# Kernel tuning notes

Hardware: AMD Instinct MI355X
Metric: run time of the kernel (lower is better)

The kernel has to match this reference:

```python
import jax, jax.numpy as jnp
import numpy as np

T, B, IN, H, L = 512, 256, 64, 128, 5  # seq, batch, in_dim, hidden, layers


def _lstm_layer(x_seq, W_ih, W_hh, b_ih, b_hh):
    # x_seq: [T, B, D]; W_ih: [4H, D]; W_hh: [4H, H]; biases: [4H]
    # Precompute input contribution for all timesteps (big GEMM, compute-dense)
    pre = jnp.einsum('tbd,gd->tbg', x_seq, W_ih) + b_ih + b_hh  # [T, B, 4H]
    h0 = jnp.zeros((x_seq.shape[1], W_hh.shape[1]), x_seq.dtype)
    c0 = h0

    def step(carry, p):
        h, c = carry
        gates = p + h @ W_hh.T  # [B, 4H], PyTorch gate order i,f,g,o
        i, f, g, o = jnp.split(gates, 4, axis=-1)
        i = jax.nn.sigmoid(i)
        f = jax.nn.sigmoid(f)
        g = jnp.tanh(g)
        o = jax.nn.sigmoid(o)
        c = f * c + i * g
        h = o * jnp.tanh(c)
        return (h, c), h

    _, hs = jax.lax.scan(step, (h0, c0), pre)
    return hs  # [T, B, H]


def setup_inputs() -> dict:
    key = jax.random.key(0)
    ks = jax.random.split(key, 6)
    s = 1.0 / np.sqrt(H)  # PyTorch LSTM init scale
    return {
        'x': jax.random.normal(ks[0], (T, B, IN), jnp.float32),
        'W_ih0': jax.random.uniform(ks[1], (4 * H, IN), jnp.float32, -s, s),
        'W_ih_rest': jax.random.uniform(ks[2], (L - 1, 4 * H, H), jnp.float32, -s, s),
        'W_hh': jax.random.uniform(ks[3], (L, 4 * H, H), jnp.float32, -s, s),
        'b_ih': jax.random.uniform(ks[4], (L, 4 * H), jnp.float32, -s, s),
        'b_hh': jax.random.uniform(ks[5], (L, 4 * H), jnp.float32, -s, s),
    }


def reference(x, W_ih0, W_ih_rest, W_hh, b_ih, b_hh):
    # 5-layer stacked LSTM, eval mode (inter-layer dropout inactive).
    h = _lstm_layer(x, W_ih0, W_hh[0], b_ih[0], b_hh[0])
    for l in range(1, L):  # fixed small layer loop
        h = _lstm_layer(h, W_ih_rest[l - 1], W_hh[l], b_ih[l], b_hh[l])
    return h  # [T, B, H]
```

## Files before the change

### kernel.cpp

```cpp
#include <hip/hip_runtime.h>


typedef unsigned short ushort_t;
typedef unsigned int uint_t;
typedef unsigned long long ull_t;
typedef __attribute__((ext_vector_type(8))) short short8;
typedef __attribute__((ext_vector_type(4))) float floatx4;
typedef __attribute__((ext_vector_type(2))) float floatx2;

#define T_STEPS 512
#define BATCH   256
#define HID     128
#define NL      5
#define NBG     16
#define RING_R  64
#define PRIME   24
#define FLAG_STRIDE 16
#define SLOT_U  (BATCH * HID / 2)
#define RING_U  ((size_t)RING_R * SLOT_U)
#define WS_NEED (8192 + 4 * RING_U * 4)
#define LDS_BYTES 98304

__device__ __forceinline__ ushort_t f2bf(float f) {
  unsigned int u = __float_as_uint(f);
  u += 0x7FFF + ((u >> 16) & 1);
  return (ushort_t)(u >> 16);
}
__device__ __forceinline__ float sigm(float x) {
  float e = __builtin_amdgcn_exp2f(-1.442695041f * x);
  return __builtin_amdgcn_rcpf(1.0f + e);
}
__device__ __forceinline__ float tanh_(float x) {
  float e = __builtin_amdgcn_exp2f(-2.885390082f * x);
  float s = __builtin_amdgcn_rcpf(1.0f + e);
  return __builtin_fmaf(2.0f, s, -1.0f);
}
__device__ __forceinline__ int flag_ld(const int* p) {
  return __hip_atomic_load(p, __ATOMIC_RELAXED, __HIP_MEMORY_SCOPE_AGENT);
}
__device__ __forceinline__ ull_t ring_ld8(const uint_t* base, int tid) {
  return __hip_atomic_load((const ull_t*)base + tid, __ATOMIC_RELAXED,
                           __HIP_MEMORY_SCOPE_AGENT);
}
__device__ __forceinline__ void ring_st8(uint_t* base, int tid, ull_t v) {
  __hip_atomic_store((ull_t*)base + tid, v, __ATOMIC_RELAXED,
                     __HIP_MEMORY_SCOPE_AGENT);
}

__global__ void init_flags(int* flags) {
  int i = blockIdx.x * 256 + threadIdx.x;
  if (i < NL * NBG * FLAG_STRIDE)
    __hip_atomic_store(&flags[i], 0, __ATOMIC_RELAXED,
                       __HIP_MEMORY_SCOPE_AGENT);
}

template <int KIN, bool SRC_F32, bool RING_OUT>
__device__ __forceinline__ void lstm_stage(
    unsigned char* lds,
    const float* xf32,
    const uint_t* ring_in,
    const float* __restrict__ Wih, const float* __restrict__ Whh,
    const float* __restrict__ bih, const float* __restrict__ bhh,
    uint_t* ring_out,
    float* out_f32,
    int* up_flag, int* down_flag, int* my_flag, int bg)
{
  constexpr int KX = KIN / 32, KT = KX + 4;
  constexpr int XS = KIN + 8;
  constexpr int HS = 128 + 8;

  typedef ushort_t (*XT)[16][XS];
  typedef ushort_t (*HT)[16][HS];
  XT Xr = (XT)lds;
  HT Hr = (HT)(lds + (size_t)8 * 16 * XS * 2);
  int* upm = (int*)(lds + (size_t)8 * 16 * XS * 2 + (size_t)2 * 16 * HS * 2);
  int* dnm = upm + 4;

  const int tid  = threadIdx.x;
  const int wave = tid >> 6;
  const int lane = tid & 63;
  const int col  = lane & 15;
  const int quad = lane >> 4;
  const int j    = wave * 16 + col;
  const int frow = tid >> 5;
  const int fc   = tid & 31;

  for (int i = tid; i < 2 * 16 * HS; i += 512) (&Hr[0][0][0])[i] = 0;
  if (tid == 0) {
#pragma unroll
    for (int i = 0; i < 4; ++i) { upm[i] = 0; dnm[i] = 0; }
  }

  short8 wf[4][KT];
#pragma unroll
  for (int nt = 0; nt < 4; ++nt) {
    int n = nt * 128 + j;
#pragma unroll
    for (int kt = 0; kt < KX; ++kt) {
      const float* p = Wih + n * KIN + kt * 32 + quad * 8;
      short8 w;
#pragma unroll
      for (int e = 0; e < 8; ++e) w[e] = (short)f2bf(p[e]);
      wf[nt][kt] = w;
    }
#pragma unroll
    for (int kt = 0; kt < 4; ++kt) {
      const float* p = Whh + n * 128 + kt * 32 + quad * 8;
      short8 w;
#pragma unroll
      for (int e = 0; e < 8; ++e) w[e] = (short)f2bf(p[e]);
      wf[nt][KX + kt] = w;
    }
  }
  const float bi  = bih[j]       + bhh[j];
  const float bf_ = bih[128 + j] + bhh[128 + j];
  const float bgi = bih[256 + j] + bhh[256 + j];
  const float bo  = bih[384 + j] + bhh[384 + j];

  floatx4 c = {0.f, 0.f, 0.f, 0.f};
  int pu = 0, pd = 0;
  ull_t  pf4[4];
  floatx2 px4[4];
  floatx4 pA[4], pB[4];

  __syncthreads();

  if constexpr (!SRC_F32) {
    int v = 0;
    while ((v = flag_ld(up_flag)) < PRIME) __builtin_amdgcn_s_sleep(1);
    asm volatile("" ::: "memory");
    if (tid == 0) {
#pragma unroll
      for (int i = 0; i < 4; ++i) upm[i] = v;
      pu = v;
    }
    ull_t pr[8];
#pragma unroll
    for (int s = 0; s < 8; ++s)
      pr[s] = ring_ld8(ring_in + (size_t)s * SLOT_U + bg * 1024, tid);
#pragma unroll
    for (int s = 0; s < 8; ++s)
      *(ull_t*)(&Xr[s][frow][fc * 4]) = pr[s];
  } else {
    floatx2 pr[8];
#pragma unroll
    for (int s = 0; s < 8; ++s)
      pr[s] = *(const floatx2*)(xf32 +
                                ((size_t)s * BATCH + bg * 16 + frow) * 64 +
                                fc * 2);
#pragma unroll
    for (int s = 0; s < 8; ++s)
      *(uint_t*)(&Xr[s][frow][fc * 2]) =
          (uint_t)f2bf(pr[s][0]) | ((uint_t)f2bf(pr[s][1]) << 16);
  }
  asm volatile("s_waitcnt lgkmcnt(0)\n\ts_barrier" ::: "memory");

  pA[0] = (floatx4){bi, bi, bi, bi};
  pA[1] = (floatx4){bf_, bf_, bf_, bf_};
  pA[2] = (floatx4){bgi, bgi, bgi, bgi};
  pA[3] = (floatx4){bo, bo, bo, bo};
#pragma unroll
  for (int kt = 0; kt < KX; ++kt) {
    short8 ax = *(const short8*)(&Xr[0][col][kt * 32 + quad * 8]);
    pA[0] = __builtin_amdgcn_mfma_f32_16x16x32_bf16(ax, wf[0][kt], pA[0], 0, 0, 0);
    pA[1] = __builtin_amdgcn_mfma_f32_16x16x32_bf16(ax, wf[1][kt], pA[1], 0, 0, 0);
    pA[2] = __builtin_amdgcn_mfma_f32_16x16x32_bf16(ax, wf[2][kt], pA[2], 0, 0, 0);
    pA[3] = __builtin_amdgcn_mfma_f32_16x16x32_bf16(ax, wf[3][kt], pA[3], 0, 0, 0);
  }

  auto body = [&](int t, floatx4 (&pc)[4], floatx4 (&pn)[4]) {
    if ((t & 3) == 0) {
      if (t >= 4) {
        asm volatile("s_waitcnt vmcnt(0)\n\ts_barrier" ::: "memory");
        if (tid == 0)
          __hip_atomic_store(my_flag, t - 1, __ATOMIC_RELAXED,
                             __HIP_MEMORY_SCOPE_AGENT);
#pragma unroll
        for (int g = 0; g < 4; ++g) {
          const int s = t + 4 + g;
          if (s < T_STEPS) {
            if constexpr (SRC_F32)
              *(uint_t*)(&Xr[s & 7][frow][fc * 2]) =
                  (uint_t)f2bf(px4[g][0]) | ((uint_t)f2bf(px4[g][1]) << 16);
            else
              *(ull_t*)(&Xr[s & 7][frow][fc * 4]) = pf4[g];
          }
        }
      }
      if (t + 8 < T_STEPS) {
        if constexpr (!SRC_F32) {
          int need = t + 12;
          if (need > T_STEPS) need = T_STEPS;
          if (upm[t & 3] < need) {
            while (flag_ld(up_flag) < need) __builtin_amdgcn_s_sleep(1);
          }
        }
        asm volatile("" ::: "memory");
#pragma unroll
        for (int g = 0; g < 4; ++g) {
          const int s = t + 8 + g;
          if (s < T_STEPS) {
            if constexpr (SRC_F32)
              px4[g] = *(const floatx2*)(
                  xf32 + ((size_t)s * BATCH + bg * 16 + frow) * 64 + fc * 2);
            else
              pf4[g] = ring_ld8(
                  ring_in + (size_t)(s & (RING_R - 1)) * SLOT_U + bg * 1024,
                  tid);
          }
        }
      }
    }
    const int dn = dnm[t & 3];

    if constexpr (RING_OUT) {
      if (t >= 1) {
        const int s = t - 1;
        if (s - dn > RING_R - 16) {
          while (s - flag_ld(down_flag) > RING_R - 16)
            __builtin_amdgcn_s_sleep(1);
          asm volatile("" ::: "memory");
        }
        ull_t h8 = *(const ull_t*)(&Hr[t & 1][frow][fc * 4]);
        ring_st8(ring_out + (size_t)(s & (RING_R - 1)) * SLOT_U + bg * 1024,
                 tid, h8);
      }
    }

#pragma unroll
    for (int kt = 0; kt < 4; ++kt) {
      short8 a = *(const short8*)(&Hr[t & 1][col][kt * 32 + quad * 8]);
      pc[0] = __builtin_amdgcn_mfma_f32_16x16x32_bf16(a, wf[0][KX + kt], pc[0], 0, 0, 0);
      pc[1] = __builtin_amdgcn_mfma_f32_16x16x32_bf16(a, wf[1][KX + kt], pc[1], 0, 0, 0);
      pc[2] = __builtin_amdgcn_mfma_f32_16x16x32_bf16(a, wf[2][KX + kt], pc[2], 0, 0, 0);
      pc[3] = __builtin_amdgcn_mfma_f32_16x16x32_bf16(a, wf[3][KX + kt], pc[3], 0, 0, 0);
    }

    if (t + 1 < T_STEPS) {
      pn[0] = (floatx4){bi, bi, bi, bi};
      pn[1] = (floatx4){bf_, bf_, bf_, bf_};
      pn[2] = (floatx4){bgi, bgi, bgi, bgi};
      pn[3] = (floatx4){bo, bo, bo, bo};
#pragma unroll
      for (int kt = 0; kt < KX; ++kt) {
        short8 ax = *(const short8*)(&Xr[(t + 1) & 7][col][kt * 32 + quad * 8]);
        pn[0] = __builtin_amdgcn_mfma_f32_16x16x32_bf16(ax, wf[0][kt], pn[0], 0, 0, 0);
        pn[1] = __builtin_amdgcn_mfma_f32_16x16x32_bf16(ax, wf[1][kt], pn[1], 0, 0, 0);
        pn[2] = __builtin_amdgcn_mfma_f32_16x16x32_bf16(ax, wf[2][kt], pn[2], 0, 0, 0);
        pn[3] = __builtin_amdgcn_mfma_f32_16x16x32_bf16(ax, wf[3][kt], pn[3], 0, 0, 0);
      }
    }

    if (tid == 0) {
      if constexpr (!SRC_F32) {
        upm[(t + 2) & 3] = pu;
        pu = flag_ld(up_flag);
      }
      if constexpr (RING_OUT) {
        dnm[(t + 2) & 3] = pd;
        pd = flag_ld(down_flag);
      }
    }

    ushort_t (*wr)[HS] = Hr[(t & 1) ^ 1];
#pragma unroll
    for (int r = 0; r < 4; ++r) {
      float iv = sigm(pc[0][r]);
      float fv = sigm(pc[1][r]);
      float gv = tanh_(pc[2][r]);
      float ov = sigm(pc[3][r]);
      float cn = __builtin_fmaf(fv, c[r], iv * gv);
      c[r] = cn;
      float hv = ov * tanh_(cn);
      wr[quad * 4 + r][j] = f2bf(hv);
      if constexpr (!RING_OUT) {
        out_f32[((size_t)t * BATCH + bg * 16 + quad * 4 + r) * HID + j] = hv;
      }
    }

    asm volatile("s_waitcnt lgkmcnt(0)\n\ts_barrier" ::: "memory");
  };

  for (int t = 0; t < T_STEPS; t += 2) {
    body(t, pA, pB);
    body(t + 1, pB, pA);
  }

  if constexpr (RING_OUT) {
    const int s = T_STEPS - 1;
    while (s - flag_ld(down_flag) > RING_R - 16) __builtin_amdgcn_s_sleep(1);
    asm volatile("" ::: "memory");
    ull_t h8 = *(const ull_t*)(&Hr[T_STEPS & 1][frow][fc * 4]);
    ring_st8(ring_out + (size_t)(s & (RING_R - 1)) * SLOT_U + bg * 1024, tid,
             h8);
  }
  asm volatile("s_waitcnt vmcnt(0)\n\ts_barrier" ::: "memory");
  if (tid == 0)
    __hip_atomic_store(my_flag, T_STEPS, __ATOMIC_RELAXED,
                       __HIP_MEMORY_SCOPE_AGENT);
}

__global__ __launch_bounds__(512) void lstm_pipe(
    const float* x, const float* Wih0, const float* WihR,
    const float* Whh, const float* bih, const float* bhh,
    float* out, uint_t* ring, int* flags)
{
  __shared__ __align__(16) unsigned char lds_raw[LDS_BYTES];
  const int l  = blockIdx.x >> 4;
  const int bg = blockIdx.x & 15;
  int* mine = flags + (l * NBG + bg) * FLAG_STRIDE;
  int* up   = (l > 0) ? flags + ((l - 1) * NBG + bg) * FLAG_STRIDE : nullptr;
  int* down = (l < 4) ? flags + ((l + 1) * NBG + bg) * FLAG_STRIDE : nullptr;

  if (l == 0) {
    lstm_stage<64, true, true>(lds_raw, x, nullptr, Wih0, Whh, bih, bhh,
                               ring, nullptr, up, down, mine, bg);
  } else if (l < 4) {
    lstm_stage<128, false, true>(lds_raw, nullptr,
                                 ring + (size_t)(l - 1) * RING_U,
                                 WihR + (size_t)(l - 1) * 512 * 128,
                                 Whh + (size_t)l * 512 * 128,
                                 bih + l * 512, bhh + l * 512,
                                 ring + (size_t)l * RING_U, nullptr,
                                 up, down, mine, bg);
  } else {
    lstm_stage<128, false, false>(lds_raw, nullptr,
                                  ring + (size_t)3 * RING_U,
                                  WihR + (size_t)3 * 512 * 128,
                                  Whh + (size_t)4 * 512 * 128,
                                  bih + 4 * 512, bhh + 4 * 512,
                                  nullptr, out, up, nullptr, mine, bg);
  }
}

template <int KIN>
__global__ __launch_bounds__(512) void lstm_layer(
    const float* xin, float* hout,
    const float* __restrict__ Wih, const float* __restrict__ Whh,
    const float* __restrict__ bih, const float* __restrict__ bhh)
{
  constexpr int KX = KIN / 32, KT = KX + 4;
  constexpr int AW = KIN + 128, AS = AW + 8;
  constexpr int NSTG = 16 * KIN / 4;

  const int bg = blockIdx.x, tid = threadIdx.x;
  const int wave = tid >> 6, lane = tid & 63;
  const int col = lane & 15, quad = lane >> 4;
  const int j = wave * 16 + col;

  __shared__ __align__(16) ushort_t Ah[2][16][AS];
  for (int i = tid; i < 2 * 16 * AS; i += 512) (&Ah[0][0][0])[i] = 0;

  short8 wf[4][KT];
#pragma unroll
  for (int nt = 0; nt < 4; ++nt) {
    int n = nt * 128 + j;
#pragma unroll
    for (int kt = 0; kt < KX; ++kt) {
      const float* p = Wih + n * KIN + kt * 32 + quad * 8;
      short8 w;
#pragma unroll
      for (int e = 0; e < 8; ++e) w[e] = (short)f2bf(p[e]);
      wf[nt][kt] = w;
    }
#pragma unroll
    for (int kt = 0; kt < 4; ++kt) {
      const float* p = Whh + n * 128 + kt * 32 + quad * 8;
      short8 w;
#pragma unroll
      for (int e = 0; e < 8; ++e) w[e] = (short)f2bf(p[e]);
      wf[nt][KX + kt] = w;
    }
  }
  const float bi  = bih[j]       + bhh[j];
  const float bf_ = bih[128 + j] + bhh[128 + j];
  const float bgi = bih[256 + j] + bhh[256 + j];
  const float bo  = bih[384 + j] + bhh[384 + j];

  floatx4 c = {0.f, 0.f, 0.f, 0.f};
  const int srow = tid / (KIN / 4), scol = (tid % (KIN / 4)) * 4;
  floatx4 xv = {0.f, 0.f, 0.f, 0.f};
  auto stage_load = [&](int t) {
    if (tid < NSTG && t < T_STEPS)
      xv = *(const floatx4*)(xin + (size_t)(t * BATCH + bg * 16 + srow) * KIN + scol);
  };
  auto stage_store = [&](int t, ushort_t (*buf)[AS]) {
    if (tid < NSTG && t < T_STEPS) {
#pragma unroll
      for (int e = 0; e < 4; ++e) buf[srow][scol + e] = f2bf(xv[e]);
    }
  };
  __syncthreads();
  stage_load(0); stage_store(0, Ah[0]); stage_load(1);
  __syncthreads();

  for (int t = 0; t < T_STEPS; ++t) {
    ushort_t (*rd)[AS] = Ah[t & 1];
    ushort_t (*wr)[AS] = Ah[(t & 1) ^ 1];
    short8 af[KT];
#pragma unroll
    for (int kt = 0; kt < KT; ++kt)
      af[kt] = *(const short8*)(&rd[col][kt * 32 + quad * 8]);
    floatx4 a0 = {0, 0, 0, 0}, a1 = {0, 0, 0, 0}, a2 = {0, 0, 0, 0},
            a3 = {0, 0, 0, 0};
#pragma unroll
    for (int kt = 0; kt < KT; ++kt) {
      short8 a = af[kt];
      a0 = __builtin_amdgcn_mfma_f32_16x16x32_bf16(a, wf[0][kt], a0, 0, 0, 0);
      a1 = __builtin_amdgcn_mfma_f32_16x16x32_bf16(a, wf[1][kt], a1, 0, 0, 0);
      a2 = __builtin_amdgcn_mfma_f32_16x16x32_bf16(a, wf[2][kt], a2, 0, 0, 0);
      a3 = __builtin_amdgcn_mfma_f32_16x16x32_bf16(a, wf[3][kt], a3, 0, 0, 0);
    }
    stage_store(t + 1, wr);
    stage_load(t + 2);
    size_t obase = (size_t)(t * BATCH + bg * 16) * HID + j;
#pragma unroll
    for (int r = 0; r < 4; ++r) {
      int row = quad * 4 + r;
      float iv = sigm(a0[r] + bi);
      float fv = sigm(a1[r] + bf_);
      float gv = tanh_(a2[r] + bgi);
      float ov = sigm(a3[r] + bo);
      float cn = __builtin_fmaf(fv, c[r], iv * gv);
      c[r] = cn;
      float hv = ov * tanh_(cn);
      wr[row][KIN + j] = f2bf(hv);
      hout[obase + (size_t)row * HID] = hv;
    }
    __syncthreads();
  }
}

extern "C" void kernel_launch(void* const* d_in, const int* in_sizes, int n_in,
                              void* d_out, int out_size, void* d_ws,
                              size_t ws_size, hipStream_t stream) {
  const float* x    = (const float*)d_in[0];
  const float* Wih0 = (const float*)d_in[1];
  const float* WihR = (const float*)d_in[2];
  const float* Whh  = (const float*)d_in[3];
  const float* bih  = (const float*)d_in[4];
  const float* bhh  = (const float*)d_in[5];
  float* out = (float*)d_out;

  if (ws_size >= WS_NEED) {
    int* flags = (int*)d_ws;
    uint_t* ring = (uint_t*)((char*)d_ws + 8192);
    init_flags<<<(NL * NBG * FLAG_STRIDE + 255) / 256, 256, 0, stream>>>(flags);
    lstm_pipe<<<NL * NBG, 512, 0, stream>>>(x, Wih0, WihR, Whh, bih, bhh,
                                            out, ring, flags);
  } else {
    lstm_layer<64><<<16, 512, 0, stream>>>(x, out, Wih0, Whh, bih, bhh);
    for (int l = 1; l < 5; ++l)
      lstm_layer<128><<<16, 512, 0, stream>>>(
          out, out, WihR + (size_t)(l - 1) * 512 * 128,
          Whh + (size_t)l * 512 * 128, bih + l * 512, bhh + l * 512);
  }
}
```

Baseline: 863.1 us.

## Split each LSTM layer into separate input-GEMM and recurrence blocks

Adds a new pipelined kernel that uses 160 blocks. For each layer, one set of blocks computes the input projection plus bias into a global pre-activation ring, and another set runs only the recurrent h@W_hh and gate math, consuming those pre-activations. The goal is to take the input-GEMM MFMAs off the latency-critical recurrent path and overlap them on other CUs. In exchange it adds global-memory traffic for the fp32 pre-activations, more flag synchronisation between stages, and a larger workspace requirement. It falls back to the old path if the workspace is too small.

```diff
diff --git a/kernel.cpp b/kernel.cpp
--- a/kernel.cpp
+++ b/kernel.cpp
@@ -21,6 +21,15 @@
 #define WS_NEED (8192 + 4 * RING_U * 4)
 #define LDS_BYTES 98304
 
+#define HD 32
+#define PD 32
+#define HSLOT_UL 512
+#define HRING_U ((size_t)HD * 16 * 1024)
+#define PSLOT_F 8192
+#define PRING_F ((size_t)PD * 16 * PSLOT_F)
+#define WS2_FLAGS 16384
+#define WS2_NEED (WS2_FLAGS + 4 * HRING_U * 4 + 5 * PRING_F * 4)
+
 __device__ __forceinline__ ushort_t f2bf(float f) {
   unsigned int u = __float_as_uint(f);
   u += 0x7FFF + ((u >> 16) & 1);
@@ -38,43 +47,37 @@
 __device__ __forceinline__ int flag_ld(const int* p) {
   return __hip_atomic_load(p, __ATOMIC_RELAXED, __HIP_MEMORY_SCOPE_AGENT);
 }
-__device__ __forceinline__ ull_t ring_ld8(const uint_t* base, int tid) {
-  return __hip_atomic_load((const ull_t*)base + tid, __ATOMIC_RELAXED,
-                           __HIP_MEMORY_SCOPE_AGENT);
-}
-__device__ __forceinline__ void ring_st8(uint_t* base, int tid, ull_t v) {
-  __hip_atomic_store((ull_t*)base + tid, v, __ATOMIC_RELAXED,
-                     __HIP_MEMORY_SCOPE_AGENT);
+__device__ __forceinline__ void flag_st(int* p, int v) {
+  __hip_atomic_store(p, v, __ATOMIC_RELAXED, __HIP_MEMORY_SCOPE_AGENT);
+}
+__device__ __forceinline__ ull_t a_ld8(const ull_t* p) {
+  return __hip_atomic_load(p, __ATOMIC_RELAXED, __HIP_MEMORY_SCOPE_AGENT);
+}
+__device__ __forceinline__ void a_st8(ull_t* p, ull_t v) {
+  __hip_atomic_store(p, v, __ATOMIC_RELAXED, __HIP_MEMORY_SCOPE_AGENT);
 }
 
 __global__ void init_flags(int* flags) {
   int i = blockIdx.x * 256 + threadIdx.x;
   if (i < NL * NBG * FLAG_STRIDE)
-    __hip_atomic_store(&flags[i], 0, __ATOMIC_RELAXED,
-                       __HIP_MEMORY_SCOPE_AGENT);
-}
-
-template <int KIN, bool SRC_F32, bool RING_OUT>
-__device__ __forceinline__ void lstm_stage(
-    unsigned char* lds,
-    const float* xf32,
-    const uint_t* ring_in,
-    const float* __restrict__ Wih, const float* __restrict__ Whh,
+    flag_st(&flags[i], 0);
+}
+__global__ void init_flags2(int* flags) {
+  int i = blockIdx.x * 256 + threadIdx.x;
+  if (i < 4096) flag_st(&flags[i], 0);
+}
+
+template <int KIN, bool SRC_F32>
+__device__ __forceinline__ void gemm_stage2(
+    unsigned char* lds, const float* xf32, const uint_t* hring_in,
+    const float* __restrict__ Wih,
     const float* __restrict__ bih, const float* __restrict__ bhh,
-    uint_t* ring_out,
-    float* out_f32,
-    int* up_flag, int* down_flag, int* my_flag, int bg)
+    float* pre_l, int* up_flag, int* guard_flag, int* my_flag, int bg)
 {
-  constexpr int KX = KIN / 32, KT = KX + 4;
+  constexpr int KX = KIN / 32;
   constexpr int XS = KIN + 8;
-  constexpr int HS = 128 + 8;
-
   typedef ushort_t (*XT)[16][XS];
-  typedef ushort_t (*HT)[16][HS];
-  XT Xr = (XT)lds;
-  HT Hr = (HT)(lds + (size_t)8 * 16 * XS * 2);
-  int* upm = (int*)(lds + (size_t)8 * 16 * XS * 2 + (size_t)2 * 16 * HS * 2);
-  int* dnm = upm + 4;
+  XT Hb = (XT)lds;
 
   const int tid  = threadIdx.x;
   const int wave = tid >> 6;
@@ -85,13 +88,354 @@
   const int frow = tid >> 5;
   const int fc   = tid & 31;
 
+  short8 wf[4][KX];
+#pragma unroll
+  for (int nt = 0; nt < 4; ++nt) {
+    int n = nt * 128 + j;
+#pragma unroll
+    for (int kt = 0; kt < KX; ++kt) {
+      const float* p = Wih + n * KIN + kt * 32 + quad * 8;
+      short8 w;
+#pragma unroll
+      for (int e = 0; e < 8; ++e) w[e] = (short)f2bf(p[e]);
+      wf[nt][kt] = w;
+    }
+  }
+  float b4[4];
+#pragma unroll
+  for (int nt = 0; nt < 4; ++nt) b4[nt] = bih[nt * 128 + j] + bhh[nt * 128 + j];
+
+  ull_t hp0 = 0, hp1 = 0;
+  floatx2 xp0 = {0.f, 0.f}, xp1 = {0.f, 0.f};
+
+  auto src_load = [&](int s, ull_t& hu, floatx2& xu) {
+    if (s < T_STEPS) {
+      if constexpr (SRC_F32)
+        xu = *(const floatx2*)(xf32 + ((size_t)s * BATCH + bg * 16 + frow) * 64 +
+                               fc * 2);
+      else
+        hu = a_ld8((const ull_t*)(hring_in +
+                                  ((size_t)(s & (HD - 1)) * 16 + bg) * 1024) +
+                   tid);
+    }
+  };
+  auto commit = [&](int s, ull_t hu, floatx2 xu) {
+    if (s < T_STEPS) {
+      if constexpr (SRC_F32)
+        *(uint_t*)(&Hb[s & 3][frow][fc * 2]) =
+            (uint_t)f2bf(xu[0]) | ((uint_t)f2bf(xu[1]) << 16);
+      else
+        *(ull_t*)(&Hb[s & 3][frow][fc * 4]) = hu;
+    }
+  };
+
+  int avail = 0;
+  auto upwait = [&](int need) {
+    if constexpr (!SRC_F32) {
+      if (need > T_STEPS) need = T_STEPS;
+      if (avail < need) {
+        while ((avail = flag_ld(up_flag)) < need) __builtin_amdgcn_s_sleep(1);
+      }
+      asm volatile("" ::: "memory");
+    }
+  };
+
+  auto slotbody = [&](int s) {
+    short8 af[KX];
+#pragma unroll
+    for (int kt = 0; kt < KX; ++kt)
+      af[kt] = *(const short8*)(&Hb[s & 3][col][kt * 32 + quad * 8]);
+    floatx4 pn[4];
+#pragma unroll
+    for (int nt = 0; nt < 4; ++nt)
+      pn[nt] = (floatx4){b4[nt], b4[nt], b4[nt], b4[nt]};
+#pragma unroll
+    for (int kt = 0; kt < KX; ++kt) {
+      short8 a = af[kt];
+      pn[0] = __builtin_amdgcn_mfma_f32_16x16x32_bf16(a, wf[0][kt], pn[0], 0, 0, 0);
+      pn[1] = __builtin_amdgcn_mfma_f32_16x16x32_bf16(a, wf[1][kt], pn[1], 0, 0, 0);
+      pn[2] = __builtin_amdgcn_mfma_f32_16x16x32_bf16(a, wf[2][kt], pn[2], 0, 0, 0);
+      pn[3] = __builtin_amdgcn_mfma_f32_16x16x32_bf16(a, wf[3][kt], pn[3], 0, 0, 0);
+    }
+    ull_t* d = (ull_t*)(pre_l + ((size_t)(s & (PD - 1)) * 16 + bg) * PSLOT_F) +
+               tid * 8;
+#pragma unroll
+    for (int k = 0; k < 8; ++k) {
+      ull_t v = (ull_t)__float_as_uint(pn[k >> 1][(k & 1) * 2]) |
+                ((ull_t)__float_as_uint(pn[k >> 1][(k & 1) * 2 + 1]) << 32);
+      a_st8(d + k, v);
+    }
+  };
+
+  __syncthreads();
+
+  upwait(2);
+  {
+    ull_t a = 0, b = 0; floatx2 xa = {0.f, 0.f}, xb = {0.f, 0.f};
+    src_load(0, a, xa); src_load(1, b, xb);
+    commit(0, a, xa);   commit(1, b, xb);
+  }
+  upwait(4);
+  src_load(2, hp0, xp0); src_load(3, hp1, xp1);
+  asm volatile("s_waitcnt lgkmcnt(0)\n\ts_barrier" ::: "memory");
+
+  int rguard = 0;
+  for (int sp = 0; sp < 256; ++sp) {
+    const int s0 = 2 * sp;
+    if ((sp & 1) == 0 && sp) {
+      asm volatile("s_waitcnt vmcnt(0)\n\ts_barrier" ::: "memory");
+      if (tid == 0) flag_st(my_flag, s0);
+      if (s0 + 3 - rguard > PD - 8) {
+        while (s0 + 3 - (rguard = flag_ld(guard_flag)) > PD - 8)
+          __builtin_amdgcn_s_sleep(1);
+        asm volatile("" ::: "memory");
+      }
+    }
+    slotbody(s0);
+    slotbody(s0 + 1);
+    commit(s0 + 2, hp0, xp0);
+    commit(s0 + 3, hp1, xp1);
+    upwait(s0 + 6);
+    src_load(s0 + 4, hp0, xp0);
+    src_load(s0 + 5, hp1, xp1);
+    asm volatile("s_waitcnt lgkmcnt(0)\n\ts_barrier" ::: "memory");
+  }
+  asm volatile("s_waitcnt vmcnt(0)\n\ts_barrier" ::: "memory");
+  if (tid == 0) flag_st(my_flag, T_STEPS);
+}
+
+template <bool RING_OUT>
+__device__ __forceinline__ void rec_stage2(
+    unsigned char* lds, const float* pre_l, const float* __restrict__ Whh,
+    uint_t* ring_out, float* out_f32,
+    int* up_flag, int* down_flag, int* my_flag, int bg)
+{
+  constexpr int HS = 136;
+  typedef ushort_t (*HT)[16][HS];
+  HT Hr = (HT)lds;
+  int* upm = (int*)(lds + (size_t)2 * 16 * HS * 2);
+  int* dnm = upm + 4;
+
+  const int tid  = threadIdx.x;
+  const int wave = tid >> 6;
+  const int lane = tid & 63;
+  const int col  = lane & 15;
+  const int quad = lane >> 4;
+  const int j    = wave * 16 + col;
+  const int frow = tid >> 5;
+  const int fc   = tid & 31;
+
   for (int i = tid; i < 2 * 16 * HS; i += 512) (&Hr[0][0][0])[i] = 0;
   if (tid == 0) {
 #pragma unroll
     for (int i = 0; i < 4; ++i) { upm[i] = 0; dnm[i] = 0; }
   }
 
-  short8 wf[4][KT];
+  short8 wf[4][4];
+#pragma unroll
+  for (int nt = 0; nt < 4; ++nt) {
+    int n = nt * 128 + j;
+#pragma unroll
+    for (int kt = 0; kt < 4; ++kt) {
+      const float* p = Whh + n * 128 + kt * 32 + quad * 8;
+      short8 w;
+#pragma unroll
+      for (int e = 0; e < 8; ++e) w[e] = (short)f2bf(p[e]);
+      wf[nt][kt] = w;
+    }
+  }
+
+  floatx4 c = {0.f, 0.f, 0.f, 0.f};
+  int pu = 0, pd = 0;
+  floatx4 pg0[4], pg1[4], pg2[4], pg3[4];
+
+  auto load_pg = [&](int u, floatx4 (&p)[4]) {
+    const ull_t* p8 =
+        (const ull_t*)(pre_l + ((size_t)(u & (PD - 1)) * 16 + bg) * PSLOT_F) +
+        tid * 8;
+    ull_t v[8];
+#pragma unroll
+    for (int k = 0; k < 8; ++k) v[k] = a_ld8(p8 + k);
+#pragma unroll
+    for (int k = 0; k < 8; ++k) {
+      p[k >> 1][(k & 1) * 2]     = __uint_as_float((uint_t)v[k]);
+      p[k >> 1][(k & 1) * 2 + 1] = __uint_as_float((uint_t)(v[k] >> 32));
+    }
+  };
+
+  __syncthreads();
+
+  {
+    int v = 0;
+    while ((v = flag_ld(up_flag)) < 12) __builtin_amdgcn_s_sleep(1);
+    asm volatile("" ::: "memory");
+    if (tid == 0) {
+#pragma unroll
+      for (int i = 0; i < 4; ++i) upm[i] = v;
+      pu = v;
+    }
+  }
+  load_pg(0, pg0); load_pg(1, pg1); load_pg(2, pg2); load_pg(3, pg3);
+  asm volatile("s_waitcnt lgkmcnt(0)\n\ts_barrier" ::: "memory");
+
+  auto rbody = [&](int t, floatx4 (&pc)[4]) {
+    const int dn = dnm[t & 3];
+    if constexpr (RING_OUT) {
+      if (t >= 1) {
+        const int s = t - 1;
+        if (s - dn > HD - 8) {
+          while (s - flag_ld(down_flag) > HD - 8) __builtin_amdgcn_s_sleep(1);
+          asm volatile("" ::: "memory");
+        }
+        ull_t h8 = *(const ull_t*)(&Hr[t & 1][frow][fc * 4]);
+        a_st8((ull_t*)(ring_out +
+                       ((size_t)(s & (HD - 1)) * 16 + bg) * 1024) + tid,
+              h8);
+      }
+    }
+#pragma unroll
+    for (int kt = 0; kt < 4; ++kt) {
+      short8 a = *(const short8*)(&Hr[t & 1][col][kt * 32 + quad * 8]);
+      pc[0] = __builtin_amdgcn_mfma_f32_16x16x32_bf16(a, wf[0][kt], pc[0], 0, 0, 0);
+      pc[1] = __builtin_amdgcn_mfma_f32_16x16x32_bf16(a, wf[1][kt], pc[1], 0, 0, 0);
+      pc[2] = __builtin_amdgcn_mfma_f32_16x16x32_bf16(a, wf[2][kt], pc[2], 0, 0, 0);
+      pc[3] = __builtin_amdgcn_mfma_f32_16x16x32_bf16(a, wf[3][kt], pc[3], 0, 0, 0);
+    }
+    if (tid == 0) {
+      upm[(t + 2) & 3] = pu;
+      pu = flag_ld(up_flag);
+      if constexpr (RING_OUT) {
+        dnm[(t + 2) & 3] = pd;
+        pd = flag_ld(down_flag);
+      }
+    }
+    ushort_t (*wr)[HS] = Hr[(t & 1) ^ 1];
+#pragma unroll
+    for (int r = 0; r < 4; ++r) {
+      float iv = sigm(pc[0][r]);
+      float fv = sigm(pc[1][r]);
+      float gv = tanh_(pc[2][r]);
+      float ov = sigm(pc[3][r]);
+      float cn = __builtin_fmaf(fv, c[r], iv * gv);
+      c[r] = cn;
+      float hv = ov * tanh_(cn);
+      wr[quad * 4 + r][j] = f2bf(hv);
+      if constexpr (!RING_OUT) {
+        out_f32[((size_t)t * BATCH + bg * 16 + quad * 4 + r) * HID + j] = hv;
+      }
+    }
+    asm volatile("s_waitcnt lgkmcnt(0)\n\ts_barrier" ::: "memory");
+  };
+
+  auto rissue = [&](int u, floatx4 (&p)[4]) {
+    if (u < T_STEPS) {
+      const int need = u + 1;
+      const int am = upm[u & 3];
+      if (am < need) {
+        while (flag_ld(up_flag) < need) __builtin_amdgcn_s_sleep(1);
+      }
+      asm volatile("" ::: "memory");
+      load_pg(u, p);
+    }
+  };
+
+  for (int t = 0; t < T_STEPS; t += 4) {
+    asm volatile("s_waitcnt vmcnt(0)\n\ts_barrier" ::: "memory");
+    if (t && tid == 0) flag_st(my_flag, t - 1);
+    rbody(t, pg0);     rissue(t + 4, pg0);
+    rbody(t + 1, pg1); rissue(t + 5, pg1);
+    asm volatile("s_waitcnt vmcnt(0)\n\ts_barrier" ::: "memory");
+    rbody(t + 2, pg2); rissue(t + 6, pg2);
+    rbody(t + 3, pg3); rissue(t + 7, pg3);
+  }
+  asm volatile("s_waitcnt vmcnt(0)\n\ts_barrier" ::: "memory");
+  if (tid == 0) flag_st(my_flag, T_STEPS);
+}
+
+__global__ __launch_bounds__(512) void lstm_pipe2(
+    const float* x, const float* Wih0, const float* WihR,
+    const float* Whh, const float* bih, const float* bhh,
+    float* out, uint_t* hring, float* pre, int* flags)
+{
+  __shared__ __align__(16) unsigned char lds_raw[LDS_BYTES];
+  const int stage = blockIdx.x >> 4;
+  const int bg    = blockIdx.x & 15;
+  const int l     = stage >> 1;
+  int* fl = flags;
+  auto fidx = [&](int st) { return fl + (st * 16 + bg) * FLAG_STRIDE; };
+
+  if ((stage & 1) == 0) {
+    float* pre_l = pre + (size_t)l * PRING_F;
+    int* mine  = fidx(2 * l);
+    int* guard = fidx(2 * l + 1);
+    if (l == 0) {
+      gemm_stage2<64, true>(lds_raw, x, nullptr, Wih0, bih, bhh,
+                            pre_l, nullptr, guard, mine, bg);
+    } else {
+      gemm_stage2<128, false>(lds_raw, nullptr,
+                              hring + (size_t)(l - 1) * HRING_U,
+                              WihR + (size_t)(l - 1) * 512 * 128,
+                              bih + l * 512, bhh + l * 512,
+                              pre_l, fidx(2 * (l - 1) + 1), guard, mine, bg);
+    }
+  } else {
+    const float* pre_l = pre + (size_t)l * PRING_F;
+    int* mine = fidx(2 * l + 1);
+    int* up   = fidx(2 * l);
+    if (l < 4) {
+      rec_stage2<true>(lds_raw, pre_l, Whh + (size_t)l * 512 * 128,
+                       hring + (size_t)l * HRING_U, nullptr,
+                       up, fidx(2 * (l + 1)), mine, bg);
+    } else {
+      rec_stage2<false>(lds_raw, pre_l, Whh + (size_t)4 * 512 * 128,
+                        nullptr, out, up, nullptr, mine, bg);
+    }
+  }
+}
+
+__device__ __forceinline__ ull_t ring_ld8(const uint_t* base, int tid) {
+  return a_ld8((const ull_t*)base + tid);
+}
+__device__ __forceinline__ void ring_st8(uint_t* base, int tid, ull_t v) {
+  a_st8((ull_t*)base + tid, v);
+}
+
+template <int KIN, bool SRC_F32, bool RING_OUT>
+__device__ __forceinline__ void lstm_stage(
+    unsigned char* lds,
+    const float* xf32, const uint_t* ring_in,
+    const float* __restrict__ Wih, const float* __restrict__ Whh,
+    const float* __restrict__ bih, const float* __restrict__ bhh,
+    uint_t* ring_out, float* out_f32,
+    int* up_flag, int* down_flag, int* my_flag, int bg)
+{
+  constexpr int KX = KIN / 32;
+  constexpr int XS = KIN + 8;
+  constexpr int HS = 128 + 8;
+
+  typedef ushort_t (*XT)[16][XS];
+  typedef ushort_t (*HT)[16][HS];
+  XT Xr = (XT)lds;
+  HT Hr = (HT)(lds + (size_t)8 * 16 * XS * 2);
+  int* upm = (int*)(lds + (size_t)8 * 16 * XS * 2 + (size_t)2 * 16 * HS * 2);
+  int* dnm = upm + 4;
+
+  const int tid  = threadIdx.x;
+  const int wave = tid >> 6;
+  const int lane = tid & 63;
+  const int col  = lane & 15;
+  const int quad = lane >> 4;
+  const int j    = wave * 16 + col;
+  const int frow = tid >> 5;
+  const int fc   = tid & 31;
+
+  for (int i = tid; i < 2 * 16 * HS; i += 512) (&Hr[0][0][0])[i] = 0;
+  if (tid == 0) {
+#pragma unroll
+    for (int i = 0; i < 4; ++i) { upm[i] = 0; dnm[i] = 0; }
+  }
+
+  short8 wf[4][KX + 4];
 #pragma unroll
   for (int nt = 0; nt < 4; ++nt) {
     int n = nt * 128 + j;
@@ -172,9 +516,7 @@
     if ((t & 3) == 0) {
       if (t >= 4) {
         asm volatile("s_waitcnt vmcnt(0)\n\ts_barrier" ::: "memory");
-        if (tid == 0)
-          __hip_atomic_store(my_flag, t - 1, __ATOMIC_RELAXED,
-                             __HIP_MEMORY_SCOPE_AGENT);
+        if (tid == 0) flag_st(my_flag, t - 1);
 #pragma unroll
         for (int g = 0; g < 4; ++g) {
           const int s = t + 4 + g;
@@ -295,9 +637,7 @@
              h8);
   }
   asm volatile("s_waitcnt vmcnt(0)\n\ts_barrier" ::: "memory");
-  if (tid == 0)
-    __hip_atomic_store(my_flag, T_STEPS, __ATOMIC_RELAXED,
-                       __HIP_MEMORY_SCOPE_AGENT);
+  if (tid == 0) flag_st(my_flag, T_STEPS);
 }
 
 __global__ __launch_bounds__(512) void lstm_pipe(
@@ -442,7 +782,14 @@
   const float* bhh  = (const float*)d_in[5];
   float* out = (float*)d_out;
 
-  if (ws_size >= WS_NEED) {
+  if (ws_size >= WS2_NEED) {
+    int* flags = (int*)d_ws;
+    uint_t* hring = (uint_t*)((char*)d_ws + WS2_FLAGS);
+    float* pre = (float*)((char*)d_ws + WS2_FLAGS + 4 * HRING_U * 4);
+    init_flags2<<<16, 256, 0, stream>>>(flags);
+    lstm_pipe2<<<160, 512, 0, stream>>>(x, Wih0, WihR, Whh, bih, bhh,
+                                        out, hring, pre, flags);
+  } else if (ws_size >= WS_NEED) {
     int* flags = (int*)d_ws;
     uint_t* ring = (uint_t*)((char*)d_ws + 8192);
     init_flags<<<(NL * NBG * FLAG_STRIDE + 255) / 256, 256, 0, stream>>>(flags);
```

New measurement: 2.946 ms. 241% more time.
